# Kernel tuning notes

Hardware: AMD Instinct MI355X
Metric: run time of the kernel (lower is better)

## Reference

```python
import jax, jax.numpy as jnp
import numpy as np

B = 256       # batch
IN_N = 64     # in_n_capsules
CS = 16       # input_size == current spatial size (child k=1,s=1,p=0)
HID = 128     # linformer hidden_dim
OUT_N = 32    # out_n_capsules
D = 16        # in_d_capsules == out_d_capsules (pose dim)
MPD = 4       # matrix_pose_dim = sqrt(D)
EPS = 1e-5
SCALE = D ** (-0.5)  # pose_dim ** -0.5 used in routing dots


def setup_inputs() -> dict:
    key = jax.random.key(0)
    ks = jax.random.split(key, 6)
    current_pose = jax.random.normal(ks[0], (B, IN_N, CS, CS, D), jnp.float32)
    next_pose = jax.random.normal(ks[1], (B, OUT_N, D), jnp.float32)
    w_current = 0.02 * jax.random.normal(ks[2], (IN_N, MPD, MPD), jnp.float32)
    w_next = 0.02 * jax.random.normal(ks[3], (OUT_N, MPD, MPD), jnp.float32)
    E_proj = 0.02 * jax.random.normal(ks[4], (IN_N, CS * CS, HID), jnp.float32)
    ln_weight = jnp.ones((D,), jnp.float32)
    ln_bias = jnp.zeros((D,), jnp.float32)
    return {
        'current_pose': current_pose, 'next_pose': next_pose,
        'w_current': w_current, 'w_next': w_next, 'E_proj': E_proj,
        'ln_weight': ln_weight, 'ln_bias': ln_bias, 'num_iter': 1,
    }


def reference(current_pose, next_pose, w_current, w_next, E_proj, ln_weight, ln_bias, num_iter):
    # ---- child matrix-pose bilinear transform ----
    # [B*CS*CS, IN_N, 4, 4] @ [1, IN_N, 4, 4]
    cp = current_pose.reshape(B * CS * CS, IN_N, MPD, MPD)
    cp = jnp.matmul(cp, w_current[None])
    # ---- Linformer headwise projection over spatial positions ----
    cp = cp.reshape(B, D, IN_N, 1, CS * CS)
    k_val = jnp.matmul(cp, E_proj[None]).squeeze(3)        # [B, D, IN_N, HID]
    k_val = k_val.reshape(B, D, IN_N * HID).transpose(0, 2, 1)  # [B, new_n, D]
    # ---- parent matrix-pose transform of next_pose (query) ----
    q = next_pose.reshape(B, OUT_N, MPD, MPD)
    q = jnp.matmul(w_next[None], q).reshape(B, OUT_N, D)   # [B, OUT_N, D]
    # ---- dot-product routing: softmax over parent capsules (dim -2) ----
    dots = jax.nn.softmax(jnp.einsum('bje,bie->bji', q, k_val) * SCALE, axis=-2)
    cand = jnp.einsum('bji,bie->bje', dots, k_val)          # [B, OUT_N, D]
    # ---- parent matrix-pose transform of candidates ----
    cand = jnp.matmul(w_next[None], cand.reshape(B, OUT_N, MPD, MPD))
    cand = cand.reshape(B, 1, 1, OUT_N, D)[:, 0]            # squeeze(1) -> [B, 1, OUT_N, D]
    # ---- dropout(p=0) is identity; LayerNorm over last dim ----
    mu = jnp.mean(cand, axis=-1, keepdims=True)
    var = jnp.mean((cand - mu) ** 2, axis=-1, keepdims=True)
    return (cand - mu) / jnp.sqrt(var + EPS) * ln_weight + ln_bias
```

## Files before the change

kernel.cpp:

```cpp
#include <hip/hip_runtime.h>
#include <cstdint>

#define EPSF 1e-5f
#define SCALEF 0.25f

typedef __attribute__((ext_vector_type(8))) __fp16 f16x8;
typedef __attribute__((ext_vector_type(2))) __fp16 f16x2;
typedef __attribute__((ext_vector_type(4))) float f32x4;

union U4H8 { uint4 u; f16x8 v; unsigned short s[8]; };

__device__ __forceinline__ uint32_t pk2h(float a, float b){
    union { f16x2 h; uint32_t u; } c;
    c.h = __builtin_amdgcn_cvt_pkrtz(a, b);
    return c.u;
}
__device__ __forceinline__ void gload_lds16(const void* g, void* l){
    __builtin_amdgcn_global_load_lds((const __attribute__((address_space(1))) uint32_t*)g,
                                     (__attribute__((address_space(3))) uint32_t*)l, 16, 0, 0);
}


__global__ void k_fuseF(const float* __restrict__ wc, const float* __restrict__ E,
                        unsigned short* __restrict__ Ft){
    const int blk = blockIdx.x;
    const int n2 = blk >> 4, x = blk & 15;
    const int h = threadIdx.x;
    const int j = (n2 & 3) * 16 + x;
    float w[16];
#pragma unroll
    for (int t = 0; t < 16; ++t) w[t] = wc[j * 16 + t];
    const float* Eb = E + ((size_t)n2 * 256 + x * 16) * 128 + h;
    float e[16];
#pragma unroll
    for (int t = 0; t < 16; ++t) e[t] = Eb[(size_t)t * 128];
    float v[16];
#pragma unroll
    for (int dd = 0; dd < 16; ++dd){
        const int r = dd >> 2, k = dd & 3;
        float acc = 0.f;
#pragma unroll
        for (int c = 0; c < 4; ++c) acc += w[k * 4 + c] * e[r * 4 + c];
        v[dd] = acc;
    }
    uint32_t pk[8];
#pragma unroll
    for (int q = 0; q < 8; ++q) pk[q] = pk2h(v[q * 2], v[q * 2 + 1]);
    unsigned short* dst = Ft + (size_t)n2 * 32768 + (size_t)h * 256 + x * 16;
    ((uint4*)dst)[0] = make_uint4(pk[0], pk[1], pk[2], pk[3]);
    ((uint4*)dst)[1] = make_uint4(pk[4], pk[5], pk[6], pk[7]);
}

__global__ void k_q2(const float* __restrict__ npse, const float* __restrict__ wn,
                     float* __restrict__ q2g){
    const int b = blockIdx.x;
    const int t = threadIdx.x;
    const int o = t >> 4, d = t & 15, r = d >> 2, c = d & 3;
    float acc = 0.f;
#pragma unroll
    for (int k = 0; k < 4; ++k)
        acc += wn[o * 16 + r * 4 + k] * npse[((size_t)b * 32 + o) * 16 + k * 4 + c];
    q2g[(size_t)b * 512 + t] = acc * SCALEF;
}

__global__ __launch_bounds__(256, 4) void k_gemm(const float* __restrict__ cp,
                                                 const unsigned short* __restrict__ Ft,
                                                 const float* __restrict__ q2g,
                                                 float* __restrict__ Pmid){
    __shared__ __align__(16) char smem[32768];
    unsigned short (*As)[4096] = (unsigned short (*)[4096])smem;
    unsigned short (*Fs)[4096] = (unsigned short (*)[4096])(smem + 16384);
    const int tid  = threadIdx.x;
    const int lane = tid & 63;
    const int wave = tid >> 6;
    const int wm = wave >> 1, wn2 = wave & 1;
    const int l15 = lane & 15, g = lane >> 4;
    const int mtile = blockIdx.x;
    const int n2 = blockIdx.y;
    const int n2h = n2 >> 4, y = n2 & 15;

    const float* abase[4];
    int aoff[4];
#pragma unroll
    for (int p = 0; p < 4; ++p){
        const int idx = tid + p * 256;
        const int m = idx >> 3;
        const int kq = idx & 7;
        const int b = mtile * 8 + (m >> 4);
        const int i = (m & 15) * 4 + n2h;
        abase[p] = cp + (size_t)b * 262144 + (size_t)i * 4096 + (size_t)y * 256 + kq * 4;
        aoff[p] = m * 32 + (((kq >> 1) ^ ((m >> 1) & 3)) * 8) + (kq & 1) * 4;
    }
    const unsigned short* bsrc[2];
    unsigned short* bdst[2];
#pragma unroll
    for (int p = 0; p < 2; ++p){
        const int idx = tid + p * 256;
        const int h = idx >> 2;
        const int kq4 = idx & 3;
        bsrc[p] = Ft + (size_t)n2 * 32768 + (size_t)h * 256 + ((kq4 ^ ((h >> 1) & 3)) * 8);
        bdst[p] = &Fs[0][(size_t)(p * 256 + (tid & ~63)) * 8];
    }
    int afoff[4], bfoff[4];
#pragma unroll
    for (int mf = 0; mf < 4; ++mf){
        const int row = wm * 64 + mf * 16 + l15;
        afoff[mf] = row * 32 + ((g ^ ((row >> 1) & 3)) * 8);
    }
#pragma unroll
    for (int nf = 0; nf < 4; ++nf){
        const int row = wn2 * 64 + nf * 16 + l15;
        bfoff[nf] = row * 32 + ((g ^ ((row >> 1) & 3)) * 8);
    }

    f32x4 acc[4][4];
#pragma unroll
    for (int mf = 0; mf < 4; ++mf)
#pragma unroll
        for (int nf = 0; nf < 4; ++nf) acc[mf][nf] = (f32x4){0.f, 0.f, 0.f, 0.f};

    float4 av[4];
    const int FBUF = 128 * 32;
#pragma unroll
    for (int p = 0; p < 4; ++p) av[p] = *(const float4*)(abase[p]);
#pragma unroll
    for (int p = 0; p < 2; ++p) gload_lds16(bsrc[p], bdst[p]);
#pragma unroll
    for (int p = 0; p < 4; ++p){
        uint2 w2 = make_uint2(pk2h(av[p].x, av[p].y), pk2h(av[p].z, av[p].w));
        *(uint2*)(&As[0][aoff[p]]) = w2;
    }
    __syncthreads();

    for (int kt = 0; kt < 8; ++kt){
        const int cur = kt & 1;
        if (kt < 7){
#pragma unroll
            for (int p = 0; p < 4; ++p) av[p] = *(const float4*)(abase[p] + (kt + 1) * 32);
#pragma unroll
            for (int p = 0; p < 2; ++p)
                gload_lds16(bsrc[p] + (kt + 1) * 32, bdst[p] + (cur ^ 1) * FBUF);
        }
        f16x8 af[4], bfr[4];
#pragma unroll
        for (int mf = 0; mf < 4; ++mf) af[mf] = *(const f16x8*)(&As[cur][afoff[mf]]);
#pragma unroll
        for (int nf = 0; nf < 4; ++nf) bfr[nf] = *(const f16x8*)(&Fs[cur][bfoff[nf]]);
#pragma unroll
        for (int nf = 0; nf < 4; ++nf)
#pragma unroll
            for (int mf = 0; mf < 4; ++mf)
                acc[mf][nf] = __builtin_amdgcn_mfma_f32_16x16x32_f16(af[mf], bfr[nf], acc[mf][nf], 0, 0, 0);
        if (kt < 7){
            const int nxt = cur ^ 1;
#pragma unroll
            for (int p = 0; p < 4; ++p){
                uint2 w2 = make_uint2(pk2h(av[p].x, av[p].y), pk2h(av[p].z, av[p].w));
                *(uint2*)(&As[nxt][aoff[p]]) = w2;
            }
        }
        __syncthreads();
    }

    char* eb  = smem + wave * 6144;
    char* kvT = eb;
    char* wJ  = eb + 2048;
    const f32x4 zf = (f32x4){0.f, 0.f, 0.f, 0.f};
    f32x4 pvm[4][2];

#pragma unroll
    for (int mf = 0; mf < 4; ++mf){
        const int b = mtile * 8 + wm * 4 + mf;
        U4H8 aq[2];
#pragma unroll
        for (int jh = 0; jh < 2; ++jh){
            const float4 q = *(const float4*)(q2g + (size_t)b * 512
                                              + (size_t)(jh * 16 + l15) * 16 + g * 4);
            aq[jh].u = make_uint4(pk2h(q.x, q.y), pk2h(q.z, q.w), 0u, 0u);
        }
        f32x4 pv0 = zf, pv1 = zf;
#pragma unroll
        for (int nf = 0; nf < 4; ++nf){
            U4H8 B;
            B.u = make_uint4(pk2h(acc[mf][nf][0], acc[mf][nf][1]),
                             pk2h(acc[mf][nf][2], acc[mf][nf][3]), 0u, 0u);
            const int ncol2 = (nf * 16 + l15) * 2;
#pragma unroll
            for (int r = 0; r < 4; ++r){
                const int e = g * 4 + r;
                *(unsigned short*)(kvT + e * 128 + (ncol2 ^ ((e & 7) << 4))) = B.s[r];
            }
            f32x4 s0 = __builtin_amdgcn_mfma_f32_16x16x32_f16(aq[0].v, B.v, zf, 0, 0, 0);
            f32x4 s1 = __builtin_amdgcn_mfma_f32_16x16x32_f16(aq[1].v, B.v, zf, 0, 0, 0);
            float e0[4], e1[4];
#pragma unroll
            for (int r = 0; r < 4; ++r){ e0[r] = __expf(s0[r]); e1[r] = __expf(s1[r]); }
            float ts = ((e0[0] + e0[1]) + (e0[2] + e0[3]))
                     + ((e1[0] + e1[1]) + (e1[2] + e1[3]));
            ts += __shfl_xor(ts, 16);
            ts += __shfl_xor(ts, 32);
            const float dinv = 1.f / ts;
#pragma unroll
            for (int r = 0; r < 4; ++r){
                const int j0 = 4 * g + r;
                const int sw = (j0 & 7) << 4;
                *(unsigned short*)(wJ + j0 * 128 + (ncol2 ^ sw)) =
                    (unsigned short)(pk2h(e0[r] * dinv, 0.f) & 0xFFFFu);
                *(unsigned short*)(wJ + (16 + j0) * 128 + (ncol2 ^ sw)) =
                    (unsigned short)(pk2h(e1[r] * dinv, 0.f) & 0xFFFFu);
            }
        }
#pragma unroll
        for (int kb = 0; kb < 2; ++kb){
            const int cb = kb * 64 + g * 16;
            const int swl = (l15 & 7) << 4;
            U4H8 A0, A1, Bv;
            A0.u = *(const uint4*)(wJ + l15 * 128 + (cb ^ swl));
            A1.u = *(const uint4*)(wJ + (16 + l15) * 128 + (cb ^ swl));
            Bv.u = *(const uint4*)(kvT + l15 * 128 + (cb ^ swl));
            pv0 = __builtin_amdgcn_mfma_f32_16x16x32_f16(A0.v, Bv.v, pv0, 0, 0, 0);
            pv1 = __builtin_amdgcn_mfma_f32_16x16x32_f16(A1.v, Bv.v, pv1, 0, 0, 0);
        }
        pvm[mf][0] = pv0;
        pvm[mf][1] = pv1;
    }

    __syncthreads();
    float* pvbuf = (float*)(smem + wm * 8192);
    if (wn2 == 0){
#pragma unroll
        for (int mf = 0; mf < 4; ++mf)
#pragma unroll
            for (int jh = 0; jh < 2; ++jh)
#pragma unroll
                for (int r = 0; r < 4; ++r)
                    pvbuf[mf * 512 + (jh * 16 + 4 * g + r) * 16 + l15] = pvm[mf][jh][r];
    }
    __syncthreads();
    if (wn2 == 1){
#pragma unroll
        for (int mf = 0; mf < 4; ++mf){
            const int b = mtile * 8 + wm * 4 + mf;
            float* dst = Pmid + (size_t)n2 * 131072 + (size_t)b * 512;
#pragma unroll
            for (int jh = 0; jh < 2; ++jh)
#pragma unroll
                for (int r = 0; r < 4; ++r){
                    const int idx = (jh * 16 + 4 * g + r) * 16 + l15;
                    dst[idx] = pvbuf[mf * 512 + idx] + pvm[mf][jh][r];
                }
        }
    }
}

__global__ __launch_bounds__(512) void k_fin(const float* __restrict__ Pmid,
                                             const float* __restrict__ wn,
                                             const float* __restrict__ lnw,
                                             const float* __restrict__ lnb,
                                             float* __restrict__ out){
    __shared__ float cnd[512];
    const int b = blockIdx.x, t = threadIdx.x;
    float s = 0.f;
#pragma unroll 8
    for (int n2 = 0; n2 < 64; ++n2)
        s += Pmid[(size_t)n2 * 131072 + (size_t)b * 512 + t];
    cnd[t] = s;
    __syncthreads();
    if (t < 32){
        const int o = t;
        float m2[16];
#pragma unroll
        for (int r = 0; r < 4; ++r)
#pragma unroll
            for (int c = 0; c < 4; ++c){
                float a = 0.f;
#pragma unroll
                for (int k = 0; k < 4; ++k)
                    a += wn[o * 16 + r * 4 + k] * cnd[o * 16 + k * 4 + c];
                m2[r * 4 + c] = a;
            }
        float mu = 0.f;
#pragma unroll
        for (int e = 0; e < 16; ++e) mu += m2[e];
        mu *= (1.f / 16.f);
        float var = 0.f;
#pragma unroll
        for (int e = 0; e < 16; ++e){ const float d = m2[e] - mu; var += d * d; }
        var *= (1.f / 16.f);
        const float invs = rsqrtf(var + EPSF);
#pragma unroll
        for (int e = 0; e < 16; ++e)
            out[(size_t)b * 512 + o * 16 + e] = (m2[e] - mu) * invs * lnw[e] + lnb[e];
    }
}

extern "C" void kernel_launch(void* const* d_in, const int* in_sizes, int n_in,
                              void* d_out, int out_size, void* d_ws, size_t ws_size,
                              hipStream_t stream){
    const float* cp   = (const float*)d_in[0];
    const float* npse = (const float*)d_in[1];
    const float* wc   = (const float*)d_in[2];
    const float* wn   = (const float*)d_in[3];
    const float* E    = (const float*)d_in[4];
    const float* lnw  = (const float*)d_in[5];
    const float* lnb  = (const float*)d_in[6];
    float* out = (float*)d_out;

    char* ws = (char*)d_ws;
    unsigned short* Ft   = (unsigned short*)ws;
    float*          q2g  = (float*)(ws + 4194304);
    float*          Pmid = (float*)(ws + 4718592);

    hipLaunchKernelGGL(k_fuseF, dim3(1024), dim3(128), 0, stream, wc, E, Ft);
    hipLaunchKernelGGL(k_q2,    dim3(256),  dim3(512), 0, stream, npse, wn, q2g);
    hipLaunchKernelGGL(k_gemm,  dim3(32, 64), dim3(256), 0, stream, cp, Ft, q2g, Pmid);
    hipLaunchKernelGGL(k_fin,   dim3(256),  dim3(512), 0, stream, Pmid, wn, lnw, lnb, out);
}
```

Baseline: 96.55 us.

## Merge init kernels, triple-buffer B tiles, store fp16 partials

Folds the fused-weight and query-transform kernels into one launch to cut launch overhead. The GEMM main loop now triple-buffers the B (Ft) tile in LDS with a prefetch distance of two, and replaces __syncthreads with explicit waitcnt plus s_barrier so loads stay in flight. Per-block partial sums are written as fp16 instead of fp32, halving Pmid traffic in the final reduction kernel. The fp16 partials add rounding error to the 64-way sum, and the larger LDS footprint may reduce occupancy.

```diff
diff --git a/kernel.cpp b/kernel.cpp
--- a/kernel.cpp
+++ b/kernel.cpp
@@ -9,6 +9,7 @@
 typedef __attribute__((ext_vector_type(4))) float f32x4;
 
 union U4H8 { uint4 u; f16x8 v; unsigned short s[8]; };
+union U1H2 { unsigned u; f16x2 h; };
 
 __device__ __forceinline__ uint32_t pk2h(float a, float b){
     union { f16x2 h; uint32_t u; } c;
@@ -21,53 +22,57 @@
 }
 
 
-__global__ void k_fuseF(const float* __restrict__ wc, const float* __restrict__ E,
-                        unsigned short* __restrict__ Ft){
+__global__ void k_init(const float* __restrict__ wc, const float* __restrict__ E,
+                       const float* __restrict__ npse, const float* __restrict__ wnx,
+                       unsigned short* __restrict__ Ft, float* __restrict__ q2g){
     const int blk = blockIdx.x;
-    const int n2 = blk >> 4, x = blk & 15;
-    const int h = threadIdx.x;
-    const int j = (n2 & 3) * 16 + x;
-    float w[16];
-#pragma unroll
-    for (int t = 0; t < 16; ++t) w[t] = wc[j * 16 + t];
-    const float* Eb = E + ((size_t)n2 * 256 + x * 16) * 128 + h;
-    float e[16];
-#pragma unroll
-    for (int t = 0; t < 16; ++t) e[t] = Eb[(size_t)t * 128];
-    float v[16];
-#pragma unroll
-    for (int dd = 0; dd < 16; ++dd){
-        const int r = dd >> 2, k = dd & 3;
-        float acc = 0.f;
-#pragma unroll
-        for (int c = 0; c < 4; ++c) acc += w[k * 4 + c] * e[r * 4 + c];
-        v[dd] = acc;
-    }
-    uint32_t pk[8];
-#pragma unroll
-    for (int q = 0; q < 8; ++q) pk[q] = pk2h(v[q * 2], v[q * 2 + 1]);
-    unsigned short* dst = Ft + (size_t)n2 * 32768 + (size_t)h * 256 + x * 16;
-    ((uint4*)dst)[0] = make_uint4(pk[0], pk[1], pk[2], pk[3]);
-    ((uint4*)dst)[1] = make_uint4(pk[4], pk[5], pk[6], pk[7]);
-}
-
-__global__ void k_q2(const float* __restrict__ npse, const float* __restrict__ wn,
-                     float* __restrict__ q2g){
-    const int b = blockIdx.x;
-    const int t = threadIdx.x;
-    const int o = t >> 4, d = t & 15, r = d >> 2, c = d & 3;
-    float acc = 0.f;
-#pragma unroll
-    for (int k = 0; k < 4; ++k)
-        acc += wn[o * 16 + r * 4 + k] * npse[((size_t)b * 32 + o) * 16 + k * 4 + c];
-    q2g[(size_t)b * 512 + t] = acc * SCALEF;
+    const int tid = threadIdx.x;
+    if (blk < 1024){
+        const int n2 = blk >> 4, x = blk & 15;
+        const int h = tid;
+        const int j = (n2 & 3) * 16 + x;
+        float w[16];
+#pragma unroll
+        for (int t = 0; t < 16; ++t) w[t] = wc[j * 16 + t];
+        const float* Eb = E + ((size_t)n2 * 256 + x * 16) * 128 + h;
+        float e[16];
+#pragma unroll
+        for (int t = 0; t < 16; ++t) e[t] = Eb[(size_t)t * 128];
+        float v[16];
+#pragma unroll
+        for (int dd = 0; dd < 16; ++dd){
+            const int r = dd >> 2, k = dd & 3;
+            float acc = 0.f;
+#pragma unroll
+            for (int c = 0; c < 4; ++c) acc += w[k * 4 + c] * e[r * 4 + c];
+            v[dd] = acc;
+        }
+        uint32_t pk[8];
+#pragma unroll
+        for (int q = 0; q < 8; ++q) pk[q] = pk2h(v[q * 2], v[q * 2 + 1]);
+        unsigned short* dst = Ft + (size_t)n2 * 32768 + (size_t)h * 256 + x * 16;
+        ((uint4*)dst)[0] = make_uint4(pk[0], pk[1], pk[2], pk[3]);
+        ((uint4*)dst)[1] = make_uint4(pk[4], pk[5], pk[6], pk[7]);
+    } else {
+        const int b = blk - 1024;
+#pragma unroll
+        for (int q = 0; q < 4; ++q){
+            const int t = q * 128 + tid;
+            const int o = t >> 4, d = t & 15, r = d >> 2, c = d & 3;
+            float acc = 0.f;
+#pragma unroll
+            for (int k = 0; k < 4; ++k)
+                acc += wnx[o * 16 + r * 4 + k] * npse[((size_t)b * 32 + o) * 16 + k * 4 + c];
+            q2g[(size_t)b * 512 + t] = acc * SCALEF;
+        }
+    }
 }
 
 __global__ __launch_bounds__(256, 4) void k_gemm(const float* __restrict__ cp,
                                                  const unsigned short* __restrict__ Ft,
                                                  const float* __restrict__ q2g,
-                                                 float* __restrict__ Pmid){
-    __shared__ __align__(16) char smem[32768];
+                                                 unsigned short* __restrict__ Pmid){
+    __shared__ __align__(16) char smem[40960];
     unsigned short (*As)[4096] = (unsigned short (*)[4096])smem;
     unsigned short (*Fs)[4096] = (unsigned short (*)[4096])(smem + 16384);
     const int tid  = threadIdx.x;
@@ -120,11 +125,12 @@
         for (int nf = 0; nf < 4; ++nf) acc[mf][nf] = (f32x4){0.f, 0.f, 0.f, 0.f};
 
     float4 av[4];
-    const int FBUF = 128 * 32;
+#pragma unroll
+    for (int p = 0; p < 2; ++p) gload_lds16(bsrc[p], bdst[p]);
+#pragma unroll
+    for (int p = 0; p < 2; ++p) gload_lds16(bsrc[p] + 32, bdst[p] + 4096);
 #pragma unroll
     for (int p = 0; p < 4; ++p) av[p] = *(const float4*)(abase[p]);
-#pragma unroll
-    for (int p = 0; p < 2; ++p) gload_lds16(bsrc[p], bdst[p]);
 #pragma unroll
     for (int p = 0; p < 4; ++p){
         uint2 w2 = make_uint2(pk2h(av[p].x, av[p].y), pk2h(av[p].z, av[p].w));
@@ -132,34 +138,39 @@
     }
     __syncthreads();
 
+#pragma unroll
     for (int kt = 0; kt < 8; ++kt){
-        const int cur = kt & 1;
         if (kt < 7){
 #pragma unroll
             for (int p = 0; p < 4; ++p) av[p] = *(const float4*)(abase[p] + (kt + 1) * 32);
+        }
+        __builtin_amdgcn_sched_barrier(0);
+        if (kt < 6){
 #pragma unroll
             for (int p = 0; p < 2; ++p)
-                gload_lds16(bsrc[p] + (kt + 1) * 32, bdst[p] + (cur ^ 1) * FBUF);
+                gload_lds16(bsrc[p] + (kt + 2) * 32, bdst[p] + ((kt + 2) % 3) * 4096);
         }
         f16x8 af[4], bfr[4];
 #pragma unroll
-        for (int mf = 0; mf < 4; ++mf) af[mf] = *(const f16x8*)(&As[cur][afoff[mf]]);
-#pragma unroll
-        for (int nf = 0; nf < 4; ++nf) bfr[nf] = *(const f16x8*)(&Fs[cur][bfoff[nf]]);
+        for (int mf = 0; mf < 4; ++mf) af[mf] = *(const f16x8*)(&As[kt & 1][afoff[mf]]);
+#pragma unroll
+        for (int nf = 0; nf < 4; ++nf) bfr[nf] = *(const f16x8*)(&Fs[kt % 3][bfoff[nf]]);
 #pragma unroll
         for (int nf = 0; nf < 4; ++nf)
 #pragma unroll
             for (int mf = 0; mf < 4; ++mf)
                 acc[mf][nf] = __builtin_amdgcn_mfma_f32_16x16x32_f16(af[mf], bfr[nf], acc[mf][nf], 0, 0, 0);
         if (kt < 7){
-            const int nxt = cur ^ 1;
 #pragma unroll
             for (int p = 0; p < 4; ++p){
                 uint2 w2 = make_uint2(pk2h(av[p].x, av[p].y), pk2h(av[p].z, av[p].w));
-                *(uint2*)(&As[nxt][aoff[p]]) = w2;
+                *(uint2*)(&As[(kt + 1) & 1][aoff[p]]) = w2;
             }
         }
-        __syncthreads();
+        if (kt < 6){ asm volatile("s_waitcnt vmcnt(2) lgkmcnt(0)" ::: "memory"); }
+        else       { asm volatile("s_waitcnt vmcnt(0) lgkmcnt(0)" ::: "memory"); }
+        __builtin_amdgcn_s_barrier();
+        __builtin_amdgcn_sched_barrier(0);
     }
 
     char* eb  = smem + wave * 6144;
@@ -241,30 +252,35 @@
 #pragma unroll
         for (int mf = 0; mf < 4; ++mf){
             const int b = mtile * 8 + wm * 4 + mf;
-            float* dst = Pmid + (size_t)n2 * 131072 + (size_t)b * 512;
+            unsigned short* dst = Pmid + (size_t)n2 * 131072 + (size_t)b * 512;
 #pragma unroll
             for (int jh = 0; jh < 2; ++jh)
 #pragma unroll
                 for (int r = 0; r < 4; ++r){
                     const int idx = (jh * 16 + 4 * g + r) * 16 + l15;
-                    dst[idx] = pvbuf[mf * 512 + idx] + pvm[mf][jh][r];
+                    const float sum = pvbuf[mf * 512 + idx] + pvm[mf][jh][r];
+                    dst[idx] = (unsigned short)(pk2h(sum, 0.f) & 0xFFFFu);
                 }
         }
     }
 }
 
-__global__ __launch_bounds__(512) void k_fin(const float* __restrict__ Pmid,
+__global__ __launch_bounds__(256) void k_fin(const unsigned* __restrict__ Pmid,
                                              const float* __restrict__ wn,
                                              const float* __restrict__ lnw,
                                              const float* __restrict__ lnb,
                                              float* __restrict__ out){
     __shared__ float cnd[512];
     const int b = blockIdx.x, t = threadIdx.x;
-    float s = 0.f;
+    float s0 = 0.f, s1 = 0.f;
 #pragma unroll 8
-    for (int n2 = 0; n2 < 64; ++n2)
-        s += Pmid[(size_t)n2 * 131072 + (size_t)b * 512 + t];
-    cnd[t] = s;
+    for (int n2 = 0; n2 < 64; ++n2){
+        U1H2 c; c.u = Pmid[(size_t)n2 * 65536 + (size_t)b * 256 + t];
+        s0 += (float)c.h[0];
+        s1 += (float)c.h[1];
+    }
+    cnd[2 * t]     = s0;
+    cnd[2 * t + 1] = s1;
     __syncthreads();
     if (t < 32){
         const int o = t;
@@ -309,10 +325,9 @@
     char* ws = (char*)d_ws;
     unsigned short* Ft   = (unsigned short*)ws;
     float*          q2g  = (float*)(ws + 4194304);
-    float*          Pmid = (float*)(ws + 4718592);
-
-    hipLaunchKernelGGL(k_fuseF, dim3(1024), dim3(128), 0, stream, wc, E, Ft);
-    hipLaunchKernelGGL(k_q2,    dim3(256),  dim3(512), 0, stream, npse, wn, q2g);
-    hipLaunchKernelGGL(k_gemm,  dim3(32, 64), dim3(256), 0, stream, cp, Ft, q2g, Pmid);
-    hipLaunchKernelGGL(k_fin,   dim3(256),  dim3(512), 0, stream, Pmid, wn, lnw, lnb, out);
-}
+    unsigned short* Pmid = (unsigned short*)(ws + 4718592);
+
+    hipLaunchKernelGGL(k_init, dim3(1280), dim3(128), 0, stream, wc, E, npse, wn, Ft, q2g);
+    hipLaunchKernelGGL(k_gemm, dim3(32, 64), dim3(256), 0, stream, cp, Ft, q2g, Pmid);
+    hipLaunchKernelGGL(k_fin,  dim3(256), dim3(256), 0, stream, (const unsigned*)Pmid, wn, lnw, lnb, out);
+}
```

New measurement: 81.60 us, median of 3. 15.5% less time.
